# Kernel optimization log

Hardware: AMD Instinct MI355X
Metric: run time of the kernel (lower is better)

The kernel has to match this reference:

```python
import jax, jax.numpy as jnp
import numpy as np


def setup_inputs() -> dict:
    key = jax.random.key(0)
    B, T, D, H = 64, 512, 1024, 1024
    ks = jax.random.split(key, 14)
    s = 1.0 / np.sqrt(D)  # torch nn.Linear init scale
    u = lambda k, shape: jax.random.uniform(k, shape, jnp.float32, -s, s)
    return {
        "x": jax.random.normal(ks[0], (B, T, D), jnp.float32),
        "h0": jnp.zeros((B, 1, H), jnp.float32),
        "Wfz": u(ks[1], (H, D)), "bfz": u(ks[2], (H,)),
        "Wfr": u(ks[3], (H, D)), "bfr": u(ks[4], (H,)),
        "Wfh": u(ks[5], (H, D)), "bfh": u(ks[6], (H,)),
        "Wuz": u(ks[7], (H, H)), "buz": u(ks[8], (H,)),
        "Wur": u(ks[9], (H, H)), "bur": u(ks[10], (H,)),
        "Wuh": u(ks[11], (H, H)), "buh": u(ks[12], (H,)),
        "chunk_size": 1,
    }


def reference(x, h0, Wfz, bfz, Wfr, bfr, Wfh, bfh, Wuz, buz, Wur, bur, Wuh, buh, chunk_size):
    # Input-side projections are time-independent: batch them over the whole
    # sequence (same math as applying fz/fr/fh per step).
    Xz = x @ Wfz.T + bfz  # [B,T,H]
    Xr = x @ Wfr.T + bfr
    Xh = x @ Wfh.T + bfh

    def step(h, xs):  # h: [B,H]
        xz, xr, xh = xs
        z = jax.nn.sigmoid(xz + h @ Wuz.T + buz)
        r = jax.nn.sigmoid(xr + h @ Wur.T + bur)
        h_hat = jax.nn.silu(xh + (r * h) @ Wuh.T + buh)
        h = (1.0 - z) * h + z * h_hat
        return h, h

    xs = (Xz.transpose(1, 0, 2), Xr.transpose(1, 0, 2), Xh.transpose(1, 0, 2))  # [T,B,H]
    h_last, ys = jax.lax.scan(step, h0[:, 0, :], xs)
    y = ys.transpose(1, 0, 2)  # [B,T,H]
    return y, h_last[:, None, :]
```

## Files before the change

kernel.cpp:

```cpp
#include <hip/hip_runtime.h>
#include <hip/hip_bf16.h>

typedef short s16x8 __attribute__((ext_vector_type(8)));
typedef float f32x4 __attribute__((ext_vector_type(4)));

__device__ __forceinline__ float bf2f(unsigned short s) {
  union { unsigned int u; float f; } c; c.u = ((unsigned int)s) << 16; return c.f;
}
__device__ __forceinline__ short f2bf(float f) {
  union { float f; unsigned int u; } c; c.f = f;
  unsigned int r = (c.u + 0x7fffu + ((c.u >> 16) & 1u)) >> 16;
  return (short)(unsigned short)r;
}
__device__ __forceinline__ float sigm(float x) { return 1.0f / (1.0f + __expf(-x)); }

__device__ __forceinline__ void gload_lds16(const short* g, short* l) {
  __builtin_amdgcn_global_load_lds((const __attribute__((address_space(1))) void*)g,
                                   (__attribute__((address_space(3))) void*)l, 16, 0, 0);
}

__device__ __forceinline__ void cload8(const short* p,
    s16x8& d0, s16x8& d1, s16x8& d2, s16x8& d3,
    s16x8& d4, s16x8& d5, s16x8& d6, s16x8& d7)
{
  asm volatile(
    "global_load_dwordx4 %0, %[p], off sc0 sc1\n\t"
    "global_load_dwordx4 %1, %[p], off offset:64 sc0 sc1\n\t"
    "global_load_dwordx4 %2, %[p], off offset:128 sc0 sc1\n\t"
    "global_load_dwordx4 %3, %[p], off offset:192 sc0 sc1\n\t"
    "global_load_dwordx4 %4, %[p], off offset:256 sc0 sc1\n\t"
    "global_load_dwordx4 %5, %[p], off offset:320 sc0 sc1\n\t"
    "global_load_dwordx4 %6, %[p], off offset:384 sc0 sc1\n\t"
    "global_load_dwordx4 %7, %[p], off offset:448 sc0 sc1"
    : "=&v"(d0), "=&v"(d1), "=&v"(d2), "=&v"(d3),
      "=&v"(d4), "=&v"(d5), "=&v"(d6), "=&v"(d7)
    : [p]"v"(p) : "memory");
}

__global__ void prep(const float* __restrict__ x,
                     const float* __restrict__ Wfz, const float* __restrict__ Wfr, const float* __restrict__ Wfh,
                     const float* __restrict__ Wuz, const float* __restrict__ Wur, const float* __restrict__ Wuh,
                     const float* __restrict__ h0,
                     short* __restrict__ xb, short* __restrict__ Wf, short* __restrict__ Wzr,
                     short* __restrict__ Wh, short* __restrict__ hb)
{
  const long NX = 33554432L;
  const long NW = 1048576L;
  const long TOT = NX + 6*NW + 65536L;
  long stride = (long)gridDim.x * blockDim.x;
  for (long p = (long)blockIdx.x * blockDim.x + threadIdx.x; p < TOT; p += stride) {
    if (p < NX) { xb[p] = f2bf(x[p]); }
    else if (p < NX + 3*NW) {
      long q = p - NX;
      float v = q < NW ? Wfz[q] : (q < 2*NW ? Wfr[q-NW] : Wfh[q-2*NW]);
      Wf[q] = f2bf(v);
    } else if (p < NX + 5*NW) {
      long q = p - NX - 3*NW;
      float v = q < NW ? Wuz[q] : Wur[q-NW];
      Wzr[q] = f2bf(v);
    } else if (p < NX + 6*NW) {
      long q = p - NX - 5*NW;
      Wh[q] = f2bf(Wuh[q]);
    } else {
      long q = p - NX - 6*NW;
      hb[q] = f2bf(h0[q]);
    }
  }
}

__global__ __launch_bounds__(256) void gemm_x(const short* __restrict__ A, const short* __restrict__ Bw,
    const float* __restrict__ bfz, const float* __restrict__ bfr, const float* __restrict__ bfh,
    short* __restrict__ X)
{
  constexpr int M = 32768, K = 1024;
  constexpr int BM = 128, BN = 128, BK = 32;
  __shared__ __align__(16) short As[BM*BK];
  __shared__ __align__(16) short Bs[BN*BK];
  int tid = threadIdx.x, lane = tid & 63, wid = tid >> 6;
  int bm = blockIdx.x % (M/BM), bn = blockIdx.x / (M/BM);
  int wm = wid >> 1, wn = wid & 1;

  f32x4 acc[4][4];
  for (int i = 0; i < 4; ++i) for (int j = 0; j < 4; ++j) acc[i][j] = f32x4{0.f,0.f,0.f,0.f};

  int r0 = tid >> 2,        kc0 = (tid & 3) * 8;
  int r1 = (256+tid) >> 2,  kc1 = ((256+tid) & 3) * 8;
  const short* a0 = A  + (size_t)(bm*BM + r0)*K + kc0;
  const short* a1 = A  + (size_t)(bm*BM + r1)*K + kc1;
  const short* b0 = Bw + (size_t)(bn*BN + r0)*K + kc0;
  const short* b1 = Bw + (size_t)(bn*BN + r1)*K + kc1;

  const short* abase = As + (wm*64 + (lane&15))*BK + (lane>>4)*8;
  const short* bbase = Bs + (wn*64 + (lane&15))*BK + (lane>>4)*8;

  for (int k0 = 0; k0 < K; k0 += BK) {
    __syncthreads();
    gload_lds16(a0 + k0, As + wid*512);
    gload_lds16(a1 + k0, As + 2048 + wid*512);
    gload_lds16(b0 + k0, Bs + wid*512);
    gload_lds16(b1 + k0, Bs + 2048 + wid*512);
    __syncthreads();
    s16x8 af[4], bff[4];
    for (int f = 0; f < 4; ++f) {
      af[f]  = *(const s16x8*)(abase + f*16*BK);
      bff[f] = *(const s16x8*)(bbase + f*16*BK);
    }
    for (int i = 0; i < 4; ++i)
      for (int j = 0; j < 4; ++j)
        acc[i][j] = __builtin_amdgcn_mfma_f32_16x16x32_bf16(af[i], bff[j], acc[i][j], 0, 0, 0);
  }

  int col = lane & 15, rb = (lane >> 4) * 4;
  for (int fi = 0; fi < 4; ++fi) for (int fj = 0; fj < 4; ++fj) {
    int n = bn*BN + wn*64 + fj*16 + col;
    float bias = n < 1024 ? bfz[n] : (n < 2048 ? bfr[n-1024] : bfh[n-2048]);
    f32x4 c = acc[fi][fj];
    for (int i = 0; i < 4; ++i) {
      int m = bm*BM + wm*64 + fi*16 + rb + i;
      int bb = m >> 9, tt = m & 511;
      X[((size_t)tt*64 + bb)*3072 + n] = f2bf(c[i] + bias);
    }
  }
}

#define WAITV(N) asm volatile("s_waitcnt vmcnt(" #N ")" ::: "memory"); \
                 __builtin_amdgcn_sched_barrier(0);

__global__ __launch_bounds__(64, 1) void recur(
  const short* __restrict__ X,
  const short* __restrict__ Wzr,
  const short* __restrict__ Wh,
  const float* __restrict__ h0,
  const float* __restrict__ buz, const float* __restrict__ bur, const float* __restrict__ buh,
  short* hb,
  short* rh,
  float* y, float* hlast, int* flags)
{
  constexpr int WROW = 1032;
  __shared__ __align__(16) short Wl[48 * WROW];

  int wg = blockIdx.x;
  int cg = wg & 63, bg = wg >> 6;
  int lane = threadIdx.x;
  int col = lane & 15, hi = lane >> 4;
  int rb = hi*4, kfo = hi*8;
  int j  = cg*16 + col;
  int b0 = bg*16 + rb;
  int arow = bg*16 + col;

  for (int c = lane; c < 48*128; c += 64) {
    int row = c >> 7, o16 = c & 127;
    int gc = cg*16 + (row & 15);
    const short* src = (row < 16) ? (Wzr + (size_t)gc*1024)
                     : (row < 32) ? (Wzr + (size_t)(1024+gc)*1024)
                                  : (Wh  + (size_t)gc*1024);
    *(s16x8*)(&Wl[row*WROW + o16*8]) = *(const s16x8*)(src + o16*8);
  }

  float bz = buz[j], br = bur[j], bh = buh[j];
  float hreg[4], zreg[4];
  #pragma unroll
  for (int i = 0; i < 4; ++i) hreg[i] = h0[(b0+i)*1024 + j];

  unsigned short xs[12], xn[12];
  #pragma unroll
  for (int i = 0; i < 4; ++i) {
    const unsigned short* xp = (const unsigned short*)X + ((size_t)(b0+i))*3072 + j;
    xs[i] = xp[0]; xs[4+i] = xp[1024]; xs[8+i] = xp[2048];
  }
  __syncthreads();

  const short* wlz = Wl + col*WROW + kfo;
  const short* wlr = Wl + (16+col)*WROW + kfo;
  const short* wlh = Wl + (32+col)*WROW + kfo;
  int* fslot = flags + wg*32;
  int* fpoll = flags + ((bg<<6) + lane)*32;

  int seq = 1;
  for (int t = 0; t < 512; ++t) {
    const short* hbc = hb + (t&1)*65536;
    short* hbn = hb + ((t&1)^1)*65536;

    {
      const short* ap = hbc + (size_t)arow*1024 + kfo;
      s16x8 ah[32];
      cload8(ap,     ah[0], ah[1], ah[2], ah[3], ah[4], ah[5], ah[6], ah[7]);
      cload8(ap+256, ah[8], ah[9], ah[10],ah[11],ah[12],ah[13],ah[14],ah[15]);
      cload8(ap+512, ah[16],ah[17],ah[18],ah[19],ah[20],ah[21],ah[22],ah[23]);
      cload8(ap+768, ah[24],ah[25],ah[26],ah[27],ah[28],ah[29],ah[30],ah[31]);
      int tn = (t+1) & 511;
      #pragma unroll
      for (int i = 0; i < 4; ++i) {
        const unsigned short* xp = (const unsigned short*)X + ((size_t)tn*64 + (b0+i))*3072 + j;
        xn[i] = xp[0]; xn[4+i] = xp[1024]; xn[8+i] = xp[2048];
      }
      f32x4 acz = {0.f,0.f,0.f,0.f}, acr = {0.f,0.f,0.f,0.f};
      WAITV(24)
      #pragma unroll
      for (int n = 0; n < 8; ++n) {
        s16x8 vz = *(const s16x8*)(wlz + n*32);
        s16x8 vr = *(const s16x8*)(wlr + n*32);
        acz = __builtin_amdgcn_mfma_f32_16x16x32_bf16(ah[n], vz, acz, 0,0,0);
        acr = __builtin_amdgcn_mfma_f32_16x16x32_bf16(ah[n], vr, acr, 0,0,0);
      }
      WAITV(16)
      #pragma unroll
      for (int n = 8; n < 16; ++n) {
        s16x8 vz = *(const s16x8*)(wlz + n*32);
        s16x8 vr = *(const s16x8*)(wlr + n*32);
        acz = __builtin_amdgcn_mfma_f32_16x16x32_bf16(ah[n], vz, acz, 0,0,0);
        acr = __builtin_amdgcn_mfma_f32_16x16x32_bf16(ah[n], vr, acr, 0,0,0);
      }
      WAITV(8)
      #pragma unroll
      for (int n = 16; n < 24; ++n) {
        s16x8 vz = *(const s16x8*)(wlz + n*32);
        s16x8 vr = *(const s16x8*)(wlr + n*32);
        acz = __builtin_amdgcn_mfma_f32_16x16x32_bf16(ah[n], vz, acz, 0,0,0);
        acr = __builtin_amdgcn_mfma_f32_16x16x32_bf16(ah[n], vr, acr, 0,0,0);
      }
      WAITV(0)
      #pragma unroll
      for (int n = 24; n < 32; ++n) {
        s16x8 vz = *(const s16x8*)(wlz + n*32);
        s16x8 vr = *(const s16x8*)(wlr + n*32);
        acz = __builtin_amdgcn_mfma_f32_16x16x32_bf16(ah[n], vz, acz, 0,0,0);
        acr = __builtin_amdgcn_mfma_f32_16x16x32_bf16(ah[n], vr, acr, 0,0,0);
      }
      #pragma unroll
      for (int i = 0; i < 4; ++i) {
        zreg[i] = sigm(bf2f(xs[i]) + acz[i] + bz);
        float r = sigm(bf2f(xs[4+i]) + acr[i] + br);
        __hip_atomic_store(rh + (b0+i)*1024 + j, f2bf(r * hreg[i]),
                           __ATOMIC_RELAXED, __HIP_MEMORY_SCOPE_AGENT);
      }
    }
    {
      asm volatile("s_waitcnt vmcnt(0)" ::: "memory");
      if (lane == 0)
        __hip_atomic_store(fslot, seq, __ATOMIC_RELAXED, __HIP_MEMORY_SCOPE_AGENT);
      int fl;
      do { fl = __hip_atomic_load(fpoll, __ATOMIC_RELAXED, __HIP_MEMORY_SCOPE_AGENT); }
      while (!__all(fl >= seq));
      ++seq;
    }

    {
      const short* ap = rh + (size_t)arow*1024 + kfo;
      s16x8 ah[32];
      cload8(ap,     ah[0], ah[1], ah[2], ah[3], ah[4], ah[5], ah[6], ah[7]);
      cload8(ap+256, ah[8], ah[9], ah[10],ah[11],ah[12],ah[13],ah[14],ah[15]);
      cload8(ap+512, ah[16],ah[17],ah[18],ah[19],ah[20],ah[21],ah[22],ah[23]);
      cload8(ap+768, ah[24],ah[25],ah[26],ah[27],ah[28],ah[29],ah[30],ah[31]);
      f32x4 ach = {0.f,0.f,0.f,0.f};
      WAITV(24)
      #pragma unroll
      for (int n = 0; n < 8; ++n) {
        s16x8 vh = *(const s16x8*)(wlh + n*32);
        ach = __builtin_amdgcn_mfma_f32_16x16x32_bf16(ah[n], vh, ach, 0,0,0);
      }
      WAITV(16)
      #pragma unroll
      for (int n = 8; n < 16; ++n) {
        s16x8 vh = *(const s16x8*)(wlh + n*32);
        ach = __builtin_amdgcn_mfma_f32_16x16x32_bf16(ah[n], vh, ach, 0,0,0);
      }
      WAITV(8)
      #pragma unroll
      for (int n = 16; n < 24; ++n) {
        s16x8 vh = *(const s16x8*)(wlh + n*32);
        ach = __builtin_amdgcn_mfma_f32_16x16x32_bf16(ah[n], vh, ach, 0,0,0);
      }
      WAITV(0)
      #pragma unroll
      for (int n = 24; n < 32; ++n) {
        s16x8 vh = *(const s16x8*)(wlh + n*32);
        ach = __builtin_amdgcn_mfma_f32_16x16x32_bf16(ah[n], vh, ach, 0,0,0);
      }
      #pragma unroll
      for (int i = 0; i < 4; ++i) {
        float s  = bf2f(xs[8+i]) + ach[i] + bh;
        float hh = s * sigm(s);
        float hn = (1.0f - zreg[i])*hreg[i] + zreg[i]*hh;
        hreg[i] = hn;
        __builtin_nontemporal_store(hn, y + ((size_t)(b0+i)*512 + t)*1024 + j);
        __hip_atomic_store(hbn + (b0+i)*1024 + j, f2bf(hn),
                           __ATOMIC_RELAXED, __HIP_MEMORY_SCOPE_AGENT);
      }
      if (t == 511) {
        #pragma unroll
        for (int i = 0; i < 4; ++i) hlast[(b0+i)*1024 + j] = hreg[i];
      }
    }
    {
      asm volatile("s_waitcnt vmcnt(0)" ::: "memory");
      if (lane == 0)
        __hip_atomic_store(fslot, seq, __ATOMIC_RELAXED, __HIP_MEMORY_SCOPE_AGENT);
      int fl;
      do { fl = __hip_atomic_load(fpoll, __ATOMIC_RELAXED, __HIP_MEMORY_SCOPE_AGENT); }
      while (!__all(fl >= seq));
      ++seq;
    }

    #pragma unroll
    for (int q = 0; q < 12; ++q) xs[q] = xn[q];
  }
}

extern "C" void kernel_launch(void* const* d_in, const int* in_sizes, int n_in,
                              void* d_out, int out_size, void* d_ws, size_t ws_size,
                              hipStream_t stream) {
  const float* x   = (const float*)d_in[0];
  const float* h0  = (const float*)d_in[1];
  const float* Wfz = (const float*)d_in[2];
  const float* bfz = (const float*)d_in[3];
  const float* Wfr = (const float*)d_in[4];
  const float* bfr = (const float*)d_in[5];
  const float* Wfh = (const float*)d_in[6];
  const float* bfh = (const float*)d_in[7];
  const float* Wuz = (const float*)d_in[8];
  const float* buz = (const float*)d_in[9];
  const float* Wur = (const float*)d_in[10];
  const float* bur = (const float*)d_in[11];
  const float* Wuh = (const float*)d_in[12];
  const float* buh = (const float*)d_in[13];

  char* ws = (char*)d_ws;
  short* Xb  = (short*)(ws);
  short* xb  = (short*)(ws + 201326592);
  short* Wf  = (short*)(ws + 268435456);
  short* Wzr = (short*)(ws + 274726912);
  short* Wh  = (short*)(ws + 278921216);
  short* hb  = (short*)(ws + 281018368);
  short* rh  = (short*)(ws + 281280512);
  int*   bar = (int*)(ws + 281411584);

  float* y = (float*)d_out;
  float* hlast = y + 33554432;

  hipMemsetAsync(bar, 0, 32768, stream);
  prep<<<2048, 256, 0, stream>>>(x, Wfz, Wfr, Wfh, Wuz, Wur, Wuh, h0, xb, Wf, Wzr, Wh, hb);
  gemm_x<<<6144, 256, 0, stream>>>(xb, Wf, bfz, bfr, bfh, Xb);
  recur<<<256, 64, 0, stream>>>(Xb, Wzr, Wh, h0, buz, bur, buh, hb, rh, y, hlast, bar);
}
```

Before: 3.804 ms.

## Use atomic counter barrier, lane-major LDS weight layout, and reorder stores after signal

Measured after the change: 3.808 ms. About the same (+0.1%).

```diff
diff --git a/kernel.cpp b/kernel.cpp
--- a/kernel.cpp
+++ b/kernel.cpp
@@ -134,10 +134,9 @@
   const float* __restrict__ buz, const float* __restrict__ bur, const float* __restrict__ buh,
   short* hb,
   short* rh,
-  float* y, float* hlast, int* flags)
+  float* y, float* hlast, int* bar)
 {
-  constexpr int WROW = 1032;
-  __shared__ __align__(16) short Wl[48 * WROW];
+  __shared__ __align__(16) short Wl[3*32*64*8];
 
   int wg = blockIdx.x;
   int cg = wg & 63, bg = wg >> 6;
@@ -148,13 +147,16 @@
   int b0 = bg*16 + rb;
   int arow = bg*16 + col;
 
-  for (int c = lane; c < 48*128; c += 64) {
-    int row = c >> 7, o16 = c & 127;
-    int gc = cg*16 + (row & 15);
-    const short* src = (row < 16) ? (Wzr + (size_t)gc*1024)
-                     : (row < 32) ? (Wzr + (size_t)(1024+gc)*1024)
-                                  : (Wh  + (size_t)gc*1024);
-    *(s16x8*)(&Wl[row*WROW + o16*8]) = *(const s16x8*)(src + o16*8);
+  {
+    const short* gbase0 = Wzr + (size_t)(cg*16 + col)*1024 + kfo;
+    const short* gbase1 = Wzr + (size_t)(1024 + cg*16 + col)*1024 + kfo;
+    const short* gbase2 = Wh  + (size_t)(cg*16 + col)*1024 + kfo;
+    #pragma unroll 4
+    for (int n = 0; n < 32; ++n) {
+      *(s16x8*)(Wl + ((0*32+n)*64 + lane)*8) = *(const s16x8*)(gbase0 + n*32);
+      *(s16x8*)(Wl + ((1*32+n)*64 + lane)*8) = *(const s16x8*)(gbase1 + n*32);
+      *(s16x8*)(Wl + ((2*32+n)*64 + lane)*8) = *(const s16x8*)(gbase2 + n*32);
+    }
   }
 
   float bz = buz[j], br = bur[j], bh = buh[j];
@@ -168,15 +170,13 @@
     const unsigned short* xp = (const unsigned short*)X + ((size_t)(b0+i))*3072 + j;
     xs[i] = xp[0]; xs[4+i] = xp[1024]; xs[8+i] = xp[2048];
   }
-  __syncthreads();
-
-  const short* wlz = Wl + col*WROW + kfo;
-  const short* wlr = Wl + (16+col)*WROW + kfo;
-  const short* wlh = Wl + (32+col)*WROW + kfo;
-  int* fslot = flags + wg*32;
-  int* fpoll = flags + ((bg<<6) + lane)*32;
-
-  int seq = 1;
+
+  const short* wlbase = Wl + lane*8;
+  int* cnt = bar + bg*64;
+  int tgt = 64;
+
+  asm volatile("s_waitcnt vmcnt(0)" ::: "memory");
+
   for (int t = 0; t < 512; ++t) {
     const short* hbc = hb + (t&1)*65536;
     short* hbn = hb + ((t&1)^1)*65536;
@@ -188,42 +188,36 @@
       cload8(ap+256, ah[8], ah[9], ah[10],ah[11],ah[12],ah[13],ah[14],ah[15]);
       cload8(ap+512, ah[16],ah[17],ah[18],ah[19],ah[20],ah[21],ah[22],ah[23]);
       cload8(ap+768, ah[24],ah[25],ah[26],ah[27],ah[28],ah[29],ah[30],ah[31]);
-      int tn = (t+1) & 511;
-      #pragma unroll
-      for (int i = 0; i < 4; ++i) {
-        const unsigned short* xp = (const unsigned short*)X + ((size_t)tn*64 + (b0+i))*3072 + j;
-        xn[i] = xp[0]; xn[4+i] = xp[1024]; xn[8+i] = xp[2048];
-      }
       f32x4 acz = {0.f,0.f,0.f,0.f}, acr = {0.f,0.f,0.f,0.f};
       WAITV(24)
       #pragma unroll
       for (int n = 0; n < 8; ++n) {
-        s16x8 vz = *(const s16x8*)(wlz + n*32);
-        s16x8 vr = *(const s16x8*)(wlr + n*32);
+        s16x8 vz = *(const s16x8*)(wlbase + n*512);
+        s16x8 vr = *(const s16x8*)(wlbase + 16384 + n*512);
         acz = __builtin_amdgcn_mfma_f32_16x16x32_bf16(ah[n], vz, acz, 0,0,0);
         acr = __builtin_amdgcn_mfma_f32_16x16x32_bf16(ah[n], vr, acr, 0,0,0);
       }
       WAITV(16)
       #pragma unroll
       for (int n = 8; n < 16; ++n) {
-        s16x8 vz = *(const s16x8*)(wlz + n*32);
-        s16x8 vr = *(const s16x8*)(wlr + n*32);
+        s16x8 vz = *(const s16x8*)(wlbase + n*512);
+        s16x8 vr = *(const s16x8*)(wlbase + 16384 + n*512);
         acz = __builtin_amdgcn_mfma_f32_16x16x32_bf16(ah[n], vz, acz, 0,0,0);
         acr = __builtin_amdgcn_mfma_f32_16x16x32_bf16(ah[n], vr, acr, 0,0,0);
       }
       WAITV(8)
       #pragma unroll
       for (int n = 16; n < 24; ++n) {
-        s16x8 vz = *(const s16x8*)(wlz + n*32);
-        s16x8 vr = *(const s16x8*)(wlr + n*32);
+        s16x8 vz = *(const s16x8*)(wlbase + n*512);
+        s16x8 vr = *(const s16x8*)(wlbase + 16384 + n*512);
         acz = __builtin_amdgcn_mfma_f32_16x16x32_bf16(ah[n], vz, acz, 0,0,0);
         acr = __builtin_amdgcn_mfma_f32_16x16x32_bf16(ah[n], vr, acr, 0,0,0);
       }
       WAITV(0)
       #pragma unroll
       for (int n = 24; n < 32; ++n) {
-        s16x8 vz = *(const s16x8*)(wlz + n*32);
-        s16x8 vr = *(const s16x8*)(wlr + n*32);
+        s16x8 vz = *(const s16x8*)(wlbase + n*512);
+        s16x8 vr = *(const s16x8*)(wlbase + 16384 + n*512);
         acz = __builtin_amdgcn_mfma_f32_16x16x32_bf16(ah[n], vz, acz, 0,0,0);
         acr = __builtin_amdgcn_mfma_f32_16x16x32_bf16(ah[n], vr, acr, 0,0,0);
       }
@@ -235,14 +229,14 @@
                            __ATOMIC_RELAXED, __HIP_MEMORY_SCOPE_AGENT);
       }
     }
+    asm volatile("s_waitcnt vmcnt(0)" ::: "memory");
+    if (lane == 0)
+      __hip_atomic_fetch_add(cnt, 1, __ATOMIC_RELAXED, __HIP_MEMORY_SCOPE_AGENT);
     {
-      asm volatile("s_waitcnt vmcnt(0)" ::: "memory");
-      if (lane == 0)
-        __hip_atomic_store(fslot, seq, __ATOMIC_RELAXED, __HIP_MEMORY_SCOPE_AGENT);
-      int fl;
-      do { fl = __hip_atomic_load(fpoll, __ATOMIC_RELAXED, __HIP_MEMORY_SCOPE_AGENT); }
-      while (!__all(fl >= seq));
-      ++seq;
+      int v;
+      do { v = __hip_atomic_load(cnt, __ATOMIC_RELAXED, __HIP_MEMORY_SCOPE_AGENT); }
+      while (v < tgt);
+      tgt += 64;
     }
 
     {
@@ -256,50 +250,59 @@
       WAITV(24)
       #pragma unroll
       for (int n = 0; n < 8; ++n) {
-        s16x8 vh = *(const s16x8*)(wlh + n*32);
+        s16x8 vh = *(const s16x8*)(wlbase + 32768 + n*512);
         ach = __builtin_amdgcn_mfma_f32_16x16x32_bf16(ah[n], vh, ach, 0,0,0);
       }
       WAITV(16)
       #pragma unroll
       for (int n = 8; n < 16; ++n) {
-        s16x8 vh = *(const s16x8*)(wlh + n*32);
+        s16x8 vh = *(const s16x8*)(wlbase + 32768 + n*512);
         ach = __builtin_amdgcn_mfma_f32_16x16x32_bf16(ah[n], vh, ach, 0,0,0);
       }
       WAITV(8)
       #pragma unroll
       for (int n = 16; n < 24; ++n) {
-        s16x8 vh = *(const s16x8*)(wlh + n*32);
+        s16x8 vh = *(const s16x8*)(wlbase + 32768 + n*512);
         ach = __builtin_amdgcn_mfma_f32_16x16x32_bf16(ah[n], vh, ach, 0,0,0);
       }
       WAITV(0)
       #pragma unroll
       for (int n = 24; n < 32; ++n) {
-        s16x8 vh = *(const s16x8*)(wlh + n*32);
+        s16x8 vh = *(const s16x8*)(wlbase + 32768 + n*512);
         ach = __builtin_amdgcn_mfma_f32_16x16x32_bf16(ah[n], vh, ach, 0,0,0);
       }
+      float hnv[4];
       #pragma unroll
       for (int i = 0; i < 4; ++i) {
         float s  = bf2f(xs[8+i]) + ach[i] + bh;
         float hh = s * sigm(s);
         float hn = (1.0f - zreg[i])*hreg[i] + zreg[i]*hh;
-        hreg[i] = hn;
-        __builtin_nontemporal_store(hn, y + ((size_t)(b0+i)*512 + t)*1024 + j);
+        hnv[i] = hn; hreg[i] = hn;
         __hip_atomic_store(hbn + (b0+i)*1024 + j, f2bf(hn),
                            __ATOMIC_RELAXED, __HIP_MEMORY_SCOPE_AGENT);
+      }
+      asm volatile("s_waitcnt vmcnt(0)" ::: "memory");
+      if (lane == 0)
+        __hip_atomic_fetch_add(cnt, 1, __ATOMIC_RELAXED, __HIP_MEMORY_SCOPE_AGENT);
+      #pragma unroll
+      for (int i = 0; i < 4; ++i)
+        __builtin_nontemporal_store(hnv[i], y + ((size_t)(b0+i)*512 + t)*1024 + j);
+      int tn = (t+1) & 511;
+      #pragma unroll
+      for (int i = 0; i < 4; ++i) {
+        const unsigned short* xp = (const unsigned short*)X + ((size_t)tn*64 + (b0+i))*3072 + j;
+        xn[i] = xp[0]; xn[4+i] = xp[1024]; xn[8+i] = xp[2048];
       }
       if (t == 511) {
         #pragma unroll
         for (int i = 0; i < 4; ++i) hlast[(b0+i)*1024 + j] = hreg[i];
       }
-    }
-    {
-      asm volatile("s_waitcnt vmcnt(0)" ::: "memory");
-      if (lane == 0)
-        __hip_atomic_store(fslot, seq, __ATOMIC_RELAXED, __HIP_MEMORY_SCOPE_AGENT);
-      int fl;
-      do { fl = __hip_atomic_load(fpoll, __ATOMIC_RELAXED, __HIP_MEMORY_SCOPE_AGENT); }
-      while (!__all(fl >= seq));
-      ++seq;
+      {
+        int v;
+        do { v = __hip_atomic_load(cnt, __ATOMIC_RELAXED, __HIP_MEMORY_SCOPE_AGENT); }
+        while (v < tgt);
+        tgt += 64;
+      }
     }
 
     #pragma unroll
@@ -338,7 +341,7 @@
   float* y = (float*)d_out;
   float* hlast = y + 33554432;
 
-  hipMemsetAsync(bar, 0, 32768, stream);
+  hipMemsetAsync(bar, 0, 1024, stream);
   prep<<<2048, 256, 0, stream>>>(x, Wfz, Wfr, Wfh, Wuz, Wur, Wuh, h0, xb, Wf, Wzr, Wh, hb);
   gemm_x<<<6144, 256, 0, stream>>>(xb, Wf, bfz, bfr, bfh, Xb);
   recur<<<256, 64, 0, stream>>>(Xb, Wzr, Wh, h0, buz, bur, buh, hb, rh, y, hlast, bar);
```
